# Kernel tuning notes

Hardware: AMD Instinct MI355X
Metric: run time of the kernel (lower is better)

Reference implementation:

```python
import jax, jax.numpy as jnp
import numpy as np
from jax import lax


def _box_filter(x, ksize):
    """Depthwise box filter (mean over ksize x ksize window) with reflect padding.
    x: [B, C, H, W] -> [B, C, H, W]
    """
    C = x.shape[1]
    p = ksize // 2
    xp = jnp.pad(x, ((0, 0), (0, 0), (p, p), (p, p)), mode='reflect')
    # depthwise kernel: (out_ch=C, in_ch/groups=1, kh, kw), uniform 1/k^2
    kernel = jnp.full((C, 1, ksize, ksize), 1.0 / (ksize * ksize), dtype=x.dtype)
    return lax.conv_general_dilated(
        xp, kernel,
        window_strides=(1, 1), padding='VALID',
        dimension_numbers=('NCHW', 'OIHW', 'NCHW'),
        feature_group_count=C,
    )


def setup_inputs() -> dict:
    key = jax.random.key(0)
    x = jax.random.normal(key, (16, 3, 1024, 1024), dtype=jnp.float32)
    return {"x": x, "ksize": 7}


def reference(x, ksize):
    local_mean = _box_filter(x, ksize)
    local_var = _box_filter(x * x, ksize) - local_mean ** 2
    # noise_power is None in this config: per (B, C) spatial mean of local variance
    noise_power = jnp.mean(local_var, axis=(2, 3), keepdims=True)  # [B, C, 1, 1]
    out = (x - local_mean) * (1.0 - noise_power / local_var) + local_mean
    out = jnp.where(local_var < noise_power, local_mean, out)
    return out
```

## Files before the change

kernel.cpp:

```cpp
#include <hip/hip_runtime.h>


#define HH 1024
#define WW 1024
#define RB 64
#define NT 256
#define NIMG 48
#define STRIPS (HH / RB)

__device__ __forceinline__ int vrefl(int i) {
    i = (i < 0) ? -i : i;
    return (i >= HH) ? (2 * HH - 2 - i) : i;
}

__device__ __forceinline__ float4 ld4(const float* p) {
    return *reinterpret_cast<const float4*>(p);
}

template <int FINAL>
__global__ __launch_bounds__(NT) void wiener_pass(const float* __restrict__ x,
                                                  float* __restrict__ nsum,
                                                  float* __restrict__ out) {
    __shared__ __align__(16) float s_cs[2][WW + 8];
    __shared__ __align__(16) float s_c2[2][WW + 8];
    __shared__ float s_red[NT / 64];

    const int t = threadIdx.x;
    const int r0 = blockIdx.x * RB;
    const int bc = blockIdx.y;
    const int c0 = t * 4;

    const float* img = x + (size_t)bc * (HH * WW);

    float csx = 0.f, csy = 0.f, csz = 0.f, csw = 0.f;
    float c2x = 0.f, c2y = 0.f, c2z = 0.f, c2w = 0.f;
#pragma unroll
    for (int k = -3; k <= 2; ++k) {
        const int rr = vrefl(r0 + k);
        float4 v = ld4(img + (size_t)rr * WW + c0);
        csx += v.x; csy += v.y; csz += v.z; csw += v.w;
        c2x = fmaf(v.x, v.x, c2x); c2y = fmaf(v.y, v.y, c2y);
        c2z = fmaf(v.z, v.z, c2z); c2w = fmaf(v.w, v.w, c2w);
    }

    float np = 0.f;
    if (FINAL) np = nsum[bc] * (1.0f / ((float)HH * (float)WW));
    float vacc = 0.f;
    const float inv = 1.0f / 49.0f;

    float* oimg = FINAL ? (out + (size_t)bc * (HH * WW)) : nullptr;

    for (int r = r0; r < r0 + RB; ++r) {
        const int p = r & 1;
        const int rN = vrefl(r + 3);
        const int rO = vrefl(r - 3);
        float4 nv = ld4(img + (size_t)rN * WW + c0);
        float4 ov = ld4(img + (size_t)rO * WW + c0);
        float4 xv;
        if (FINAL) xv = ld4(img + (size_t)r * WW + c0);

        csx += nv.x; csy += nv.y; csz += nv.z; csw += nv.w;
        c2x = fmaf(nv.x, nv.x, c2x); c2y = fmaf(nv.y, nv.y, c2y);
        c2z = fmaf(nv.z, nv.z, c2z); c2w = fmaf(nv.w, nv.w, c2w);

        float* cs = s_cs[p];
        float* c2 = s_c2[p];
        reinterpret_cast<float4*>(cs)[t + 1] = make_float4(csx, csy, csz, csw);
        reinterpret_cast<float4*>(c2)[t + 1] = make_float4(c2x, c2y, c2z, c2w);
        if (t == 0) {
            cs[0] = csx; cs[1] = csw; cs[2] = csz; cs[3] = csy;
            c2[0] = c2x; c2[1] = c2w; c2[2] = c2z; c2[3] = c2y;
        }
        if (t == NT - 1) {
            cs[4 + WW] = csz; cs[4 + WW + 1] = csy; cs[4 + WW + 2] = csx; cs[4 + WW + 3] = csw;
            c2[4 + WW] = c2z; c2[4 + WW + 1] = c2y; c2[4 + WW + 2] = c2x; c2[4 + WW + 3] = c2w;
        }
        __syncthreads();

        float4 la = reinterpret_cast<const float4*>(cs)[t];
        float4 lc = reinterpret_cast<const float4*>(cs)[t + 2];
        float4 ma = reinterpret_cast<const float4*>(c2)[t];
        float4 mc = reinterpret_cast<const float4*>(c2)[t + 2];

        float s0 = la.y + la.z + la.w + csx + csy + csz + csw;
        float s1 = s0 - la.y + lc.x;
        float s2 = s1 - la.z + lc.y;
        float s3 = s2 - la.w + lc.z;
        float q0 = ma.y + ma.z + ma.w + c2x + c2y + c2z + c2w;
        float q1 = q0 - ma.y + mc.x;
        float q2 = q1 - ma.z + mc.y;
        float q3 = q2 - ma.w + mc.z;

        float m0 = s0 * inv, m1 = s1 * inv, m2 = s2 * inv, m3 = s3 * inv;
        float v0 = fmaf(q0, inv, -m0 * m0);
        float v1 = fmaf(q1, inv, -m1 * m1);
        float v2 = fmaf(q2, inv, -m2 * m2);
        float v3 = fmaf(q3, inv, -m3 * m3);

        if (FINAL) {
            float g0 = 1.0f - np / v0;
            float g1 = 1.0f - np / v1;
            float g2 = 1.0f - np / v2;
            float g3 = 1.0f - np / v3;
            float o0 = fmaf(xv.x - m0, g0, m0);
            float o1 = fmaf(xv.y - m1, g1, m1);
            float o2 = fmaf(xv.z - m2, g2, m2);
            float o3 = fmaf(xv.w - m3, g3, m3);
            o0 = (v0 < np) ? m0 : o0;
            o1 = (v1 < np) ? m1 : o1;
            o2 = (v2 < np) ? m2 : o2;
            o3 = (v3 < np) ? m3 : o3;
            *reinterpret_cast<float4*>(oimg + (size_t)r * WW + c0) =
                make_float4(o0, o1, o2, o3);
        } else {
            vacc += (v0 + v1) + (v2 + v3);
        }

        csx -= ov.x; csy -= ov.y; csz -= ov.z; csw -= ov.w;
        c2x = fmaf(-ov.x, ov.x, c2x); c2y = fmaf(-ov.y, ov.y, c2y);
        c2z = fmaf(-ov.z, ov.z, c2z); c2w = fmaf(-ov.w, ov.w, c2w);
    }

    if (!FINAL) {
#pragma unroll
        for (int off = 32; off > 0; off >>= 1)
            vacc += __shfl_down(vacc, off, 64);
        __syncthreads();
        if ((t & 63) == 0) s_red[t >> 6] = vacc;
        __syncthreads();
        if (t == 0) {
            float b = (s_red[0] + s_red[1]) + (s_red[2] + s_red[3]);
            atomicAdd(&nsum[bc], b);
        }
    }
}

extern "C" void kernel_launch(void* const* d_in, const int* in_sizes, int n_in,
                              void* d_out, int out_size, void* d_ws, size_t ws_size,
                              hipStream_t stream) {
    const float* x = (const float*)d_in[0];
    float* out = (float*)d_out;
    float* nsum = (float*)d_ws;

    hipMemsetAsync(nsum, 0, NIMG * sizeof(float), stream);

    dim3 grid(STRIPS, NIMG);
    wiener_pass<0><<<grid, NT, 0, stream>>>(x, nsum, nullptr);
    wiener_pass<1><<<grid, NT, 0, stream>>>(x, nsum, out);
}
```

Baseline: 449.0 us.

## Compute noise power from weighted squared sums instead of box-filtered variance

In the first pass the sum of local variances is rewritten algebraically. The sum of box-filtered x² becomes a weighted sum of x² per pixel, with weights 4/7/8 that encode reflect-padding multiplicity, and from that it subtracts the sum of squared local means. This removes the squared-sum shared-memory staging and horizontal window math from the reduction pass. The output stores in the final pass also become nontemporal. The algebraic reformulation may change float rounding in the noise estimate.

```diff
diff --git a/kernel.cpp b/kernel.cpp
--- a/kernel.cpp
+++ b/kernel.cpp
@@ -8,9 +8,17 @@
 #define NIMG 48
 #define STRIPS (HH / RB)
 
+typedef float f32x4 __attribute__((ext_vector_type(4)));
+
 __device__ __forceinline__ int vrefl(int i) {
     i = (i < 0) ? -i : i;
     return (i >= HH) ? (2 * HH - 2 - i) : i;
+}
+
+__device__ __forceinline__ float wvf(int r) {
+    if (r <= 3) return (r == 0) ? 4.0f : 8.0f;
+    if (r >= HH - 4) return (r == HH - 1) ? 4.0f : 8.0f;
+    return 7.0f;
 }
 
 __device__ __forceinline__ float4 ld4(const float* p) {
@@ -22,7 +30,7 @@
                                                   float* __restrict__ nsum,
                                                   float* __restrict__ out) {
     __shared__ __align__(16) float s_cs[2][WW + 8];
-    __shared__ __align__(16) float s_c2[2][WW + 8];
+    __shared__ __align__(16) float s_c2[FINAL ? 2 : 1][WW + 8];
     __shared__ float s_red[NT / 64];
 
     const int t = threadIdx.x;
@@ -32,20 +40,31 @@
 
     const float* img = x + (size_t)bc * (HH * WW);
 
+    float whx = 7.f, why = 7.f, whz = 7.f, whw = 7.f;
+    if (t == 0) { whx = 4.f; why = 8.f; whz = 8.f; whw = 8.f; }
+    if (t == NT - 1) { whx = 8.f; why = 8.f; whz = 8.f; whw = 4.f; }
+
     float csx = 0.f, csy = 0.f, csz = 0.f, csw = 0.f;
     float c2x = 0.f, c2y = 0.f, c2z = 0.f, c2w = 0.f;
+    float sq_acc = 0.f;
 #pragma unroll
     for (int k = -3; k <= 2; ++k) {
         const int rr = vrefl(r0 + k);
         float4 v = ld4(img + (size_t)rr * WW + c0);
         csx += v.x; csy += v.y; csz += v.z; csw += v.w;
-        c2x = fmaf(v.x, v.x, c2x); c2y = fmaf(v.y, v.y, c2y);
-        c2z = fmaf(v.z, v.z, c2z); c2w = fmaf(v.w, v.w, c2w);
+        if (FINAL) {
+            c2x = fmaf(v.x, v.x, c2x); c2y = fmaf(v.y, v.y, c2y);
+            c2z = fmaf(v.z, v.z, c2z); c2w = fmaf(v.w, v.w, c2w);
+        } else if (k >= 0) {
+            float d = fmaf(v.x * v.x, whx, fmaf(v.y * v.y, why,
+                      fmaf(v.z * v.z, whz, v.w * v.w * whw)));
+            sq_acc = fmaf(d, wvf(r0 + k), sq_acc);
+        }
     }
 
     float np = 0.f;
     if (FINAL) np = nsum[bc] * (1.0f / ((float)HH * (float)WW));
-    float vacc = 0.f;
+    float msq_acc = 0.f;
     const float inv = 1.0f / 49.0f;
 
     float* oimg = FINAL ? (out + (size_t)bc * (HH * WW)) : nullptr;
@@ -60,44 +79,53 @@
         if (FINAL) xv = ld4(img + (size_t)r * WW + c0);
 
         csx += nv.x; csy += nv.y; csz += nv.z; csw += nv.w;
-        c2x = fmaf(nv.x, nv.x, c2x); c2y = fmaf(nv.y, nv.y, c2y);
-        c2z = fmaf(nv.z, nv.z, c2z); c2w = fmaf(nv.w, nv.w, c2w);
+        if (FINAL) {
+            c2x = fmaf(nv.x, nv.x, c2x); c2y = fmaf(nv.y, nv.y, c2y);
+            c2z = fmaf(nv.z, nv.z, c2z); c2w = fmaf(nv.w, nv.w, c2w);
+        } else if (r < r0 + RB - 3) {
+            float d = fmaf(nv.x * nv.x, whx, fmaf(nv.y * nv.y, why,
+                      fmaf(nv.z * nv.z, whz, nv.w * nv.w * whw)));
+            sq_acc = fmaf(d, wvf(r + 3), sq_acc);
+        }
 
         float* cs = s_cs[p];
-        float* c2 = s_c2[p];
+        float* c2 = s_c2[FINAL ? p : 0];
         reinterpret_cast<float4*>(cs)[t + 1] = make_float4(csx, csy, csz, csw);
-        reinterpret_cast<float4*>(c2)[t + 1] = make_float4(c2x, c2y, c2z, c2w);
+        if (FINAL)
+            reinterpret_cast<float4*>(c2)[t + 1] = make_float4(c2x, c2y, c2z, c2w);
         if (t == 0) {
             cs[0] = csx; cs[1] = csw; cs[2] = csz; cs[3] = csy;
-            c2[0] = c2x; c2[1] = c2w; c2[2] = c2z; c2[3] = c2y;
+            if (FINAL) { c2[0] = c2x; c2[1] = c2w; c2[2] = c2z; c2[3] = c2y; }
         }
         if (t == NT - 1) {
             cs[4 + WW] = csz; cs[4 + WW + 1] = csy; cs[4 + WW + 2] = csx; cs[4 + WW + 3] = csw;
-            c2[4 + WW] = c2z; c2[4 + WW + 1] = c2y; c2[4 + WW + 2] = c2x; c2[4 + WW + 3] = c2w;
+            if (FINAL) {
+                c2[4 + WW] = c2z; c2[4 + WW + 1] = c2y; c2[4 + WW + 2] = c2x; c2[4 + WW + 3] = c2w;
+            }
         }
         __syncthreads();
 
         float4 la = reinterpret_cast<const float4*>(cs)[t];
         float4 lc = reinterpret_cast<const float4*>(cs)[t + 2];
-        float4 ma = reinterpret_cast<const float4*>(c2)[t];
-        float4 mc = reinterpret_cast<const float4*>(c2)[t + 2];
 
         float s0 = la.y + la.z + la.w + csx + csy + csz + csw;
         float s1 = s0 - la.y + lc.x;
         float s2 = s1 - la.z + lc.y;
         float s3 = s2 - la.w + lc.z;
-        float q0 = ma.y + ma.z + ma.w + c2x + c2y + c2z + c2w;
-        float q1 = q0 - ma.y + mc.x;
-        float q2 = q1 - ma.z + mc.y;
-        float q3 = q2 - ma.w + mc.z;
-
         float m0 = s0 * inv, m1 = s1 * inv, m2 = s2 * inv, m3 = s3 * inv;
-        float v0 = fmaf(q0, inv, -m0 * m0);
-        float v1 = fmaf(q1, inv, -m1 * m1);
-        float v2 = fmaf(q2, inv, -m2 * m2);
-        float v3 = fmaf(q3, inv, -m3 * m3);
 
         if (FINAL) {
+            float4 ma = reinterpret_cast<const float4*>(c2)[t];
+            float4 mc = reinterpret_cast<const float4*>(c2)[t + 2];
+            float q0 = ma.y + ma.z + ma.w + c2x + c2y + c2z + c2w;
+            float q1 = q0 - ma.y + mc.x;
+            float q2 = q1 - ma.z + mc.y;
+            float q3 = q2 - ma.w + mc.z;
+            float v0 = fmaf(q0, inv, -m0 * m0);
+            float v1 = fmaf(q1, inv, -m1 * m1);
+            float v2 = fmaf(q2, inv, -m2 * m2);
+            float v3 = fmaf(q3, inv, -m3 * m3);
+
             float g0 = 1.0f - np / v0;
             float g1 = 1.0f - np / v1;
             float g2 = 1.0f - np / v2;
@@ -110,18 +138,25 @@
             o1 = (v1 < np) ? m1 : o1;
             o2 = (v2 < np) ? m2 : o2;
             o3 = (v3 < np) ? m3 : o3;
-            *reinterpret_cast<float4*>(oimg + (size_t)r * WW + c0) =
-                make_float4(o0, o1, o2, o3);
+            f32x4 ov4 = {o0, o1, o2, o3};
+            __builtin_nontemporal_store(ov4,
+                reinterpret_cast<f32x4*>(oimg + (size_t)r * WW + c0));
         } else {
-            vacc += (v0 + v1) + (v2 + v3);
+            msq_acc = fmaf(m0, m0, msq_acc);
+            msq_acc = fmaf(m1, m1, msq_acc);
+            msq_acc = fmaf(m2, m2, msq_acc);
+            msq_acc = fmaf(m3, m3, msq_acc);
         }
 
         csx -= ov.x; csy -= ov.y; csz -= ov.z; csw -= ov.w;
-        c2x = fmaf(-ov.x, ov.x, c2x); c2y = fmaf(-ov.y, ov.y, c2y);
-        c2z = fmaf(-ov.z, ov.z, c2z); c2w = fmaf(-ov.w, ov.w, c2w);
+        if (FINAL) {
+            c2x = fmaf(-ov.x, ov.x, c2x); c2y = fmaf(-ov.y, ov.y, c2y);
+            c2z = fmaf(-ov.z, ov.z, c2z); c2w = fmaf(-ov.w, ov.w, c2w);
+        }
     }
 
     if (!FINAL) {
+        float vacc = fmaf(sq_acc, inv, -msq_acc);
 #pragma unroll
         for (int off = 32; off > 0; off >>= 1)
             vacc += __shfl_down(vacc, off, 64);
@@ -142,7 +177,7 @@
     float* out = (float*)d_out;
     float* nsum = (float*)d_ws;
 
-    hipMemsetAsync(nsum, 0, NIMG * sizeof(float), stream);
+    (void)hipMemsetAsync(nsum, 0, NIMG * sizeof(float), stream);
 
     dim3 grid(STRIPS, NIMG);
     wiener_pass<0><<<grid, NT, 0, stream>>>(x, nsum, nullptr);
```

Result: faster. 394.5 us (-12.2%).

## Compute noise power via weighted square sums and register row ring

Applied to the files above, without the earlier changes.

Pass one no longer builds a box-filtered x² field. It gets the sum of box-filtered x² from reflect-padding multiplicity weights applied to x², and subtracts the sum of squared local means. The kernel keeps an 8-row register ring so each row is loaded once instead of re-reading the old and current rows. Per-strip partial sums replace the atomics and memset, and pass two sums them itself. Output uses nontemporal stores, and launch bounds request 3 blocks per CU. The weighted-sum identity changes floating-point summation order and adds register pressure.

```diff
diff --git a/kernel.cpp b/kernel.cpp
--- a/kernel.cpp
+++ b/kernel.cpp
@@ -8,21 +8,29 @@
 #define NIMG 48
 #define STRIPS (HH / RB)
 
+typedef float f32x4 __attribute__((ext_vector_type(4)));
+
 __device__ __forceinline__ int vrefl(int i) {
     i = (i < 0) ? -i : i;
     return (i >= HH) ? (2 * HH - 2 - i) : i;
 }
 
+__device__ __forceinline__ float wvf(int r) {
+    if (r <= 3) return (r == 0) ? 4.0f : 8.0f;
+    if (r >= HH - 4) return (r == HH - 1) ? 4.0f : 8.0f;
+    return 7.0f;
+}
+
 __device__ __forceinline__ float4 ld4(const float* p) {
     return *reinterpret_cast<const float4*>(p);
 }
 
 template <int FINAL>
-__global__ __launch_bounds__(NT) void wiener_pass(const float* __restrict__ x,
-                                                  float* __restrict__ nsum,
-                                                  float* __restrict__ out) {
+__global__ __launch_bounds__(NT, 3) void wiener_pass(const float* __restrict__ x,
+                                                     float* __restrict__ nsum,
+                                                     float* __restrict__ out) {
     __shared__ __align__(16) float s_cs[2][WW + 8];
-    __shared__ __align__(16) float s_c2[2][WW + 8];
+    __shared__ __align__(16) float s_c2[FINAL ? 2 : 1][WW + 8];
     __shared__ float s_red[NT / 64];
 
     const int t = threadIdx.x;
@@ -32,96 +40,146 @@
 
     const float* img = x + (size_t)bc * (HH * WW);
 
+    float whx = 7.f, why = 7.f, whz = 7.f, whw = 7.f;
+    if (t == 0) { whx = 4.f; why = 8.f; whz = 8.f; whw = 8.f; }
+    if (t == NT - 1) { whx = 8.f; why = 8.f; whz = 8.f; whw = 4.f; }
+
+    float4 q0, q1, q2, q3, q4, q5, q6, q7;
+    q5 = ld4(img + (size_t)vrefl(r0 - 3) * WW + c0);
+    q6 = ld4(img + (size_t)vrefl(r0 - 2) * WW + c0);
+    q7 = ld4(img + (size_t)vrefl(r0 - 1) * WW + c0);
+    q0 = ld4(img + (size_t)(r0 + 0) * WW + c0);
+    q1 = ld4(img + (size_t)(r0 + 1) * WW + c0);
+    q2 = ld4(img + (size_t)(r0 + 2) * WW + c0);
+
     float csx = 0.f, csy = 0.f, csz = 0.f, csw = 0.f;
     float c2x = 0.f, c2y = 0.f, c2z = 0.f, c2w = 0.f;
+    float sq_acc = 0.f;
+
+#define ACCROW(Q)                                                         \
+    csx += Q.x; csy += Q.y; csz += Q.z; csw += Q.w;                       \
+    if (FINAL) {                                                          \
+        c2x = fmaf(Q.x, Q.x, c2x); c2y = fmaf(Q.y, Q.y, c2y);             \
+        c2z = fmaf(Q.z, Q.z, c2z); c2w = fmaf(Q.w, Q.w, c2w);             \
+    }
+    ACCROW(q5) ACCROW(q6) ACCROW(q7) ACCROW(q0) ACCROW(q1) ACCROW(q2)
+#undef ACCROW
+    if (!FINAL) {
+#define SQROW(Q, R)                                                       \
+        {                                                                 \
+            float d = fmaf(Q.x * Q.x, whx, fmaf(Q.y * Q.y, why,           \
+                      fmaf(Q.z * Q.z, whz, Q.w * Q.w * whw)));            \
+            sq_acc = fmaf(d, wvf(R), sq_acc);                             \
+        }
+        SQROW(q0, r0) SQROW(q1, r0 + 1) SQROW(q2, r0 + 2)
+#undef SQROW
+    }
+
+    float np = 0.f;
+    if (FINAL) {
+        float s = 0.f;
 #pragma unroll
-    for (int k = -3; k <= 2; ++k) {
-        const int rr = vrefl(r0 + k);
-        float4 v = ld4(img + (size_t)rr * WW + c0);
-        csx += v.x; csy += v.y; csz += v.z; csw += v.w;
-        c2x = fmaf(v.x, v.x, c2x); c2y = fmaf(v.y, v.y, c2y);
-        c2z = fmaf(v.z, v.z, c2z); c2w = fmaf(v.w, v.w, c2w);
-    }
-
-    float np = 0.f;
-    if (FINAL) np = nsum[bc] * (1.0f / ((float)HH * (float)WW));
-    float vacc = 0.f;
+        for (int i = 0; i < STRIPS; ++i) s += nsum[bc * STRIPS + i];
+        np = s * (1.0f / ((float)HH * (float)WW));
+    }
+    float msq_acc = 0.f;
     const float inv = 1.0f / 49.0f;
 
     float* oimg = FINAL ? (out + (size_t)bc * (HH * WW)) : nullptr;
 
-    for (int r = r0; r < r0 + RB; ++r) {
-        const int p = r & 1;
-        const int rN = vrefl(r + 3);
-        const int rO = vrefl(r - 3);
-        float4 nv = ld4(img + (size_t)rN * WW + c0);
-        float4 ov = ld4(img + (size_t)rO * WW + c0);
-        float4 xv;
-        if (FINAL) xv = ld4(img + (size_t)r * WW + c0);
-
-        csx += nv.x; csy += nv.y; csz += nv.z; csw += nv.w;
-        c2x = fmaf(nv.x, nv.x, c2x); c2y = fmaf(nv.y, nv.y, c2y);
-        c2z = fmaf(nv.z, nv.z, c2z); c2w = fmaf(nv.w, nv.w, c2w);
-
-        float* cs = s_cs[p];
-        float* c2 = s_c2[p];
-        reinterpret_cast<float4*>(cs)[t + 1] = make_float4(csx, csy, csz, csw);
-        reinterpret_cast<float4*>(c2)[t + 1] = make_float4(c2x, c2y, c2z, c2w);
-        if (t == 0) {
-            cs[0] = csx; cs[1] = csw; cs[2] = csz; cs[3] = csy;
-            c2[0] = c2x; c2[1] = c2w; c2[2] = c2z; c2[3] = c2y;
-        }
-        if (t == NT - 1) {
-            cs[4 + WW] = csz; cs[4 + WW + 1] = csy; cs[4 + WW + 2] = csx; cs[4 + WW + 3] = csw;
-            c2[4 + WW] = c2z; c2[4 + WW + 1] = c2y; c2[4 + WW + 2] = c2x; c2[4 + WW + 3] = c2w;
-        }
-        __syncthreads();
-
-        float4 la = reinterpret_cast<const float4*>(cs)[t];
-        float4 lc = reinterpret_cast<const float4*>(cs)[t + 2];
-        float4 ma = reinterpret_cast<const float4*>(c2)[t];
-        float4 mc = reinterpret_cast<const float4*>(c2)[t + 2];
-
-        float s0 = la.y + la.z + la.w + csx + csy + csz + csw;
-        float s1 = s0 - la.y + lc.x;
-        float s2 = s1 - la.z + lc.y;
-        float s3 = s2 - la.w + lc.z;
-        float q0 = ma.y + ma.z + ma.w + c2x + c2y + c2z + c2w;
-        float q1 = q0 - ma.y + mc.x;
-        float q2 = q1 - ma.z + mc.y;
-        float q3 = q2 - ma.w + mc.z;
-
-        float m0 = s0 * inv, m1 = s1 * inv, m2 = s2 * inv, m3 = s3 * inv;
-        float v0 = fmaf(q0, inv, -m0 * m0);
-        float v1 = fmaf(q1, inv, -m1 * m1);
-        float v2 = fmaf(q2, inv, -m2 * m2);
-        float v3 = fmaf(q3, inv, -m3 * m3);
-
-        if (FINAL) {
-            float g0 = 1.0f - np / v0;
-            float g1 = 1.0f - np / v1;
-            float g2 = 1.0f - np / v2;
-            float g3 = 1.0f - np / v3;
-            float o0 = fmaf(xv.x - m0, g0, m0);
-            float o1 = fmaf(xv.y - m1, g1, m1);
-            float o2 = fmaf(xv.z - m2, g2, m2);
-            float o3 = fmaf(xv.w - m3, g3, m3);
-            o0 = (v0 < np) ? m0 : o0;
-            o1 = (v1 < np) ? m1 : o1;
-            o2 = (v2 < np) ? m2 : o2;
-            o3 = (v3 < np) ? m3 : o3;
-            *reinterpret_cast<float4*>(oimg + (size_t)r * WW + c0) =
-                make_float4(o0, o1, o2, o3);
-        } else {
-            vacc += (v0 + v1) + (v2 + v3);
-        }
-
-        csx -= ov.x; csy -= ov.y; csz -= ov.z; csw -= ov.w;
-        c2x = fmaf(-ov.x, ov.x, c2x); c2y = fmaf(-ov.y, ov.y, c2y);
-        c2z = fmaf(-ov.z, ov.z, c2z); c2w = fmaf(-ov.w, ov.w, c2w);
-    }
+#define ROWBODY(J, QN, QO, QX)                                                 \
+    {                                                                          \
+        const int r = rbase + (J);                                             \
+        QN = ld4(img + (size_t)vrefl(r + 3) * WW + c0);                        \
+        csx += QN.x; csy += QN.y; csz += QN.z; csw += QN.w;                    \
+        if (FINAL) {                                                           \
+            c2x = fmaf(QN.x, QN.x, c2x); c2y = fmaf(QN.y, QN.y, c2y);          \
+            c2z = fmaf(QN.z, QN.z, c2z); c2w = fmaf(QN.w, QN.w, c2w);          \
+        } else if (r < r0 + RB - 3) {                                          \
+            float d = fmaf(QN.x * QN.x, whx, fmaf(QN.y * QN.y, why,            \
+                      fmaf(QN.z * QN.z, whz, QN.w * QN.w * whw)));             \
+            sq_acc = fmaf(d, wvf(r + 3), sq_acc);                              \
+        }                                                                      \
+        float* cs = s_cs[(J) & 1];                                             \
+        float* c2 = s_c2[FINAL ? ((J) & 1) : 0];                               \
+        reinterpret_cast<float4*>(cs)[t + 1] = make_float4(csx, csy, csz, csw);\
+        if (FINAL)                                                             \
+            reinterpret_cast<float4*>(c2)[t + 1] =                             \
+                make_float4(c2x, c2y, c2z, c2w);                               \
+        if (t == 0) {                                                          \
+            cs[0] = csx; cs[1] = csw; cs[2] = csz; cs[3] = csy;                \
+            if (FINAL) { c2[0] = c2x; c2[1] = c2w; c2[2] = c2z; c2[3] = c2y; } \
+        }                                                                      \
+        if (t == NT - 1) {                                                     \
+            cs[4 + WW] = csz; cs[4 + WW + 1] = csy;                            \
+            cs[4 + WW + 2] = csx; cs[4 + WW + 3] = csw;                        \
+            if (FINAL) {                                                       \
+                c2[4 + WW] = c2z; c2[4 + WW + 1] = c2y;                        \
+                c2[4 + WW + 2] = c2x; c2[4 + WW + 3] = c2w;                    \
+            }                                                                  \
+        }                                                                      \
+        __syncthreads();                                                       \
+        float4 la = reinterpret_cast<const float4*>(cs)[t];                    \
+        float4 lc = reinterpret_cast<const float4*>(cs)[t + 2];                \
+        float s0 = la.y + la.z + la.w + csx + csy + csz + csw;                 \
+        float s1 = s0 - la.y + lc.x;                                           \
+        float s2 = s1 - la.z + lc.y;                                           \
+        float s3 = s2 - la.w + lc.z;                                           \
+        float m0 = s0 * inv, m1 = s1 * inv, m2 = s2 * inv, m3 = s3 * inv;      \
+        if (FINAL) {                                                           \
+            float4 ma = reinterpret_cast<const float4*>(c2)[t];                \
+            float4 mc = reinterpret_cast<const float4*>(c2)[t + 2];            \
+            float u0 = ma.y + ma.z + ma.w + c2x + c2y + c2z + c2w;             \
+            float u1 = u0 - ma.y + mc.x;                                       \
+            float u2 = u1 - ma.z + mc.y;                                       \
+            float u3 = u2 - ma.w + mc.z;                                       \
+            float v0 = fmaf(u0, inv, -m0 * m0);                                \
+            float v1 = fmaf(u1, inv, -m1 * m1);                                \
+            float v2 = fmaf(u2, inv, -m2 * m2);                                \
+            float v3 = fmaf(u3, inv, -m3 * m3);                                \
+            float g0 = 1.0f - np / v0;                                         \
+            float g1 = 1.0f - np / v1;                                         \
+            float g2 = 1.0f - np / v2;                                         \
+            float g3 = 1.0f - np / v3;                                         \
+            float o0 = fmaf(QX.x - m0, g0, m0);                                \
+            float o1 = fmaf(QX.y - m1, g1, m1);                                \
+            float o2 = fmaf(QX.z - m2, g2, m2);                                \
+            float o3 = fmaf(QX.w - m3, g3, m3);                                \
+            o0 = (v0 < np) ? m0 : o0;                                          \
+            o1 = (v1 < np) ? m1 : o1;                                          \
+            o2 = (v2 < np) ? m2 : o2;                                          \
+            o3 = (v3 < np) ? m3 : o3;                                          \
+            f32x4 ov4 = {o0, o1, o2, o3};                                      \
+            __builtin_nontemporal_store(ov4,                                   \
+                reinterpret_cast<f32x4*>(oimg + (size_t)r * WW + c0));         \
+        } else {                                                               \
+            msq_acc = fmaf(m0, m0, msq_acc);                                   \
+            msq_acc = fmaf(m1, m1, msq_acc);                                   \
+            msq_acc = fmaf(m2, m2, msq_acc);                                   \
+            msq_acc = fmaf(m3, m3, msq_acc);                                   \
+        }                                                                      \
+        csx -= QO.x; csy -= QO.y; csz -= QO.z; csw -= QO.w;                    \
+        if (FINAL) {                                                           \
+            c2x = fmaf(-QO.x, QO.x, c2x); c2y = fmaf(-QO.y, QO.y, c2y);        \
+            c2z = fmaf(-QO.z, QO.z, c2z); c2w = fmaf(-QO.w, QO.w, c2w);        \
+        }                                                                      \
+    }
+
+    for (int it = 0; it < RB / 8; ++it) {
+        const int rbase = r0 + it * 8;
+        ROWBODY(0, q3, q5, q0)
+        ROWBODY(1, q4, q6, q1)
+        ROWBODY(2, q5, q7, q2)
+        ROWBODY(3, q6, q0, q3)
+        ROWBODY(4, q7, q1, q4)
+        ROWBODY(5, q0, q2, q5)
+        ROWBODY(6, q1, q3, q6)
+        ROWBODY(7, q2, q4, q7)
+    }
+#undef ROWBODY
 
     if (!FINAL) {
+        float vacc = fmaf(sq_acc, inv, -msq_acc);
 #pragma unroll
         for (int off = 32; off > 0; off >>= 1)
             vacc += __shfl_down(vacc, off, 64);
@@ -130,7 +188,7 @@
         __syncthreads();
         if (t == 0) {
             float b = (s_red[0] + s_red[1]) + (s_red[2] + s_red[3]);
-            atomicAdd(&nsum[bc], b);
+            nsum[bc * STRIPS + blockIdx.x] = b;
         }
     }
 }
@@ -142,8 +200,6 @@
     float* out = (float*)d_out;
     float* nsum = (float*)d_ws;
 
-    hipMemsetAsync(nsum, 0, NIMG * sizeof(float), stream);
-
     dim3 grid(STRIPS, NIMG);
     wiener_pass<0><<<grid, NT, 0, stream>>>(x, nsum, nullptr);
     wiener_pass<1><<<grid, NT, 0, stream>>>(x, nsum, out);
```

New measurement: 379.4 us. 1.18x faster.
